# Performance work log

Measured on AMD Instinct MI355X. Metric: run time of the kernel, lower is better.

Reference implementation:

```python
import jax, jax.numpy as jnp
import numpy as np
from itertools import product

# dims
V, B, C, H, Wd = 3, 4, 64, 120, 160   # views, batch, feat2d_channel, image H/W
D3 = 96                               # feat3d_dim
G = 64                                # voxel grid side
N = 200000                            # sparse voxel count
NL = 250000                           # number of link rows
K = 27                                # 3^3 sparse-conv kernel offsets
EPS = 1e-5


def _build_kernel_map(rng):
    # unique sparse coordinates (b,x,y,z) sampled from a B*G^3 grid, sorted by linear code
    lin = np.sort(rng.choice(B * G * G * G, size=N, replace=False)).astype(np.int64)
    b = lin // (G * G * G)
    r = lin % (G * G * G)
    x = r // (G * G)
    y = (r // G) % G
    z = r % G
    in_idx = np.zeros((K, N), np.int32)
    mask = np.zeros((K, N), bool)
    for k, (dx, dy, dz) in enumerate(product((-1, 0, 1), repeat=3)):
        qx, qy, qz = x + dx, y + dy, z + dz
        inb = (qx >= 0) & (qx < G) & (qy >= 0) & (qy < G) & (qz >= 0) & (qz < G)
        qc = ((b * G + np.clip(qx, 0, G - 1)) * G + np.clip(qy, 0, G - 1)) * G + np.clip(qz, 0, G - 1)
        pos = np.clip(np.searchsorted(lin, qc), 0, N - 1)
        ok = inb & (lin[pos] == qc)
        in_idx[k] = np.where(ok, pos, 0)
        mask[k] = ok
    return jnp.asarray(in_idx), jnp.asarray(mask)


def setup_inputs() -> dict:
    rng = np.random.default_rng(0)
    key = jax.random.key(0)
    ks = jax.random.split(key, 8)
    feat_2d_all = jax.random.normal(ks[0], (V, B, C, H, Wd), jnp.float32)
    feat3d_F = jax.random.normal(ks[1], (N, D3), jnp.float32)
    # links: (NL, 4, V) = [batch_idx, v(row), u(col), valid]
    links = np.stack([
        rng.integers(0, B, (NL, V)),
        rng.integers(0, H, (NL, V)),
        rng.integers(0, Wd, (NL, V)),
        rng.integers(0, 2, (NL, V)),
    ], axis=1).astype(np.int32)
    coords_map_out = rng.permutation(N).astype(np.int32)
    coords_map_in = rng.choice(NL, N, replace=False).astype(np.int32)
    in_idx, nbr_mask = _build_kernel_map(rng)
    s = 0.05
    W1 = jax.random.normal(ks[2], (K, V * C, C), jnp.float32) * s
    W2 = jax.random.normal(ks[3], (K, C, D3), jnp.float32) * s
    W3 = jax.random.normal(ks[4], (K, 2 * D3, D3), jnp.float32) * s
    return {
        'feat_2d_all': feat_2d_all, 'feat3d_F': feat3d_F,
        'links': jnp.asarray(links),
        'coords_map_in': jnp.asarray(coords_map_in),
        'coords_map_out': jnp.asarray(coords_map_out),
        'in_idx': in_idx, 'nbr_mask': nbr_mask,
        'W1': W1, 'g1': jnp.ones((C,)), 'b1': jnp.zeros((C,)),
        'W2': W2, 'g2': jnp.ones((D3,)), 'b2': jnp.zeros((D3,)),
        'W3': W3, 'g3': jnp.ones((D3,)), 'b3': jnp.zeros((D3,)),
    }


def _sconv(x, Wk, in_idx, nbr_mask):
    # sparse 3x3x3 conv: out[i] = sum_k x[nbr(i,k)] @ Wk[k], masked where no neighbor
    out = jnp.zeros((x.shape[0], Wk.shape[-1]), x.dtype)
    for k in range(Wk.shape[0]):
        g = x[in_idx[k]] * nbr_mask[k][:, None].astype(x.dtype)
        out = out + g @ Wk[k]
    return out


def _bn_relu(x, g, b):
    mu = x.mean(axis=0)
    var = x.var(axis=0)
    return jax.nn.relu(g * (x - mu) / jnp.sqrt(var + EPS) + b)


def reference(feat_2d_all, feat3d_F, links, coords_map_in, coords_map_out,
              in_idx, nbr_mask, W1, g1, b1, W2, g2, b2, W3, g3, b3):
    n = feat3d_F.shape[0]
    v_, c = feat_2d_all.shape[0], feat_2d_all.shape[2]
    # current_links[coords_map_out] = links[coords_map_in]
    cur = jnp.zeros((n, 4, v_), links.dtype).at[coords_map_out].set(links[coords_map_in])
    bi = cur[:, 0, :].T   # (V, n)
    hi = cur[:, 1, :].T
    wi = cur[:, 2, :].T
    val = cur[:, 3, :].T
    vs = jnp.arange(v_)[:, None]
    # per-view gather from (V,B,C,H,W): advanced indices around the channel slice -> (V, n, C)
    g = feat_2d_all[vs, bi, :, hi, wi]
    g = g * val[:, :, None].astype(g.dtype)
    feat_2d_to_3d = jnp.transpose(g, (1, 0, 2)).reshape(n, v_ * c)
    # view_fusion: conv3 -> BN -> ReLU -> conv3 -> BN -> ReLU
    h = _bn_relu(_sconv(feat_2d_to_3d, W1, in_idx, nbr_mask), g1, b1)
    h = _bn_relu(_sconv(h, W2, in_idx, nbr_mask), g2, b2)
    # cat with 3d features, fuse_to_3d: conv3 -> BN -> ReLU
    cat = jnp.concatenate([feat3d_F, h], axis=-1)
    out = _bn_relu(_sconv(cat, W3, in_idx, nbr_mask), g3, b3)
    return out
```

## Files before the change

kernel.cpp:

```cpp
#include <hip/hip_runtime.h>
#include <stdint.h>


constexpr int NPT = 200000;
constexpr int KNB = 27;

typedef unsigned short u16;
typedef __attribute__((ext_vector_type(8))) short     bf16x8;
typedef __attribute__((ext_vector_type(8))) unsigned short u16x8;
typedef __attribute__((ext_vector_type(4))) float     f32x4;

static __device__ __forceinline__ u16 f2bf(float f){
  unsigned int u = __float_as_uint(f);
  unsigned int r = (u + 0x7fffu + ((u >> 16) & 1u)) >> 16;
  return (u16)r;
}
static __device__ __forceinline__ float bf2f(u16 u){
  return __uint_as_float(((unsigned int)u) << 16);
}

static __device__ __forceinline__ void gload_lds16(const void* g, void* l){
  __builtin_amdgcn_global_load_lds(
      (const __attribute__((address_space(1))) void*)g,
      (__attribute__((address_space(3))) void*)(uint32_t)(uintptr_t)l,
      16, 0, 0);
}

__global__ void detect_mask_kernel(const int* __restrict__ m32, int* __restrict__ flag){
  if (threadIdx.x == 0 && blockIdx.x == 0){
    int ok = 1;
    for (int i = 0; i < 64; ++i){ int v = m32[i]; if (v != 0 && v != 1) ok = 0; }
    *flag = ok ? 2 : 0;
  }
}

__global__ __launch_bounds__(256) void transpose2d_kernel(const float* __restrict__ in,
                                                          u16* __restrict__ out){
  __shared__ float tile[64][33];
  int bid = blockIdx.x;
  int wt = bid % 5;  int rest = bid / 5;
  int h  = rest % 120; rest /= 120;
  int b  = rest % 4;  int v = rest / 4;
  int w0 = wt * 32;
  int tx = threadIdx.x & 31;
  int ty = threadIdx.x >> 5;
  const float* ip = in + ((size_t)(v*4 + b) * 64) * 19200 + h * 160 + w0;
  #pragma unroll
  for (int cc = 0; cc < 8; ++cc){
    int c = cc * 8 + ty;
    tile[c][tx] = ip[(size_t)c * 19200 + tx];
  }
  __syncthreads();
  u16* op = out + (((size_t)(v*4 + b) * 120 + h) * 160 + w0) * 64;
  int c = threadIdx.x & 63;
  int wg = threadIdx.x >> 6;
  #pragma unroll
  for (int i = 0; i < 8; ++i){
    int w = wg + i * 4;
    op[(size_t)w * 64 + c] = f2bf(tile[c][w]);
  }
}

__global__ void wconvert_kernel(const float* __restrict__ src, u16* __restrict__ dst,
                                int cin, int coutT, int coutF, int cbase){
  int gid = blockIdx.x * 256 + threadIdx.x;
  int tot = KNB * cin * coutT;
  if (gid >= tot) return;
  int ncb = coutT / 16;
  int nkc = cin / 32;
  int e    = gid & 7;
  int lane = (gid >> 3) & 63;
  int f    = gid >> 9;
  int cb   = f % ncb;  f /= ncb;
  int kc   = f % nkc;
  int k    = f / nkc;
  int ci = kc * 32 + (lane >> 4) * 8 + e;
  int co = cbase + cb * 16 + (lane & 15);
  dst[gid] = f2bf(src[((size_t)k * cin + ci) * coutF + co]);
}

__global__ void stage_a_kernel(const u16* __restrict__ ft, const int* __restrict__ links,
                               const int* __restrict__ cmi, const int* __restrict__ cmo,
                               u16* __restrict__ x0){
  int gid = blockIdx.x * 256 + threadIdx.x;
  if (gid >= NPT * 3) return;
  int i = gid / 3;
  int v = gid - i * 3;
  int outr = cmo[i];
  int l    = cmi[i];
  int b  = links[l*12 + v];
  int h  = links[l*12 + 3 + v];
  int w  = links[l*12 + 6 + v];
  int vl = links[l*12 + 9 + v];
  u16* dst = x0 + (size_t)outr * 192 + v * 64;
  if (vl){
    const u16* src = ft + (((size_t)(v*4 + b) * 120 + h) * 160 + w) * 64;
    #pragma unroll
    for (int j = 0; j < 8; ++j) ((u16x8*)dst)[j] = ((const u16x8*)src)[j];
  } else {
    u16x8 z = {};
    #pragma unroll
    for (int j = 0; j < 8; ++j) ((u16x8*)dst)[j] = z;
  }
}

__global__ void f3convert_kernel(const float* __restrict__ src, u16* __restrict__ dst){
  long gid = (long)blockIdx.x * 256 + threadIdx.x;
  long tot8 = (long)NPT * 12;
  if (gid >= tot8) return;
  int row = (int)(gid / 12);
  int c0  = (int)(gid % 12) * 8;
  const float* s = src + (size_t)row * 96 + c0;
  u16* d = dst + (size_t)row * 192 + c0;
  #pragma unroll
  for (int j = 0; j < 8; ++j) d[j] = f2bf(s[j]);
}

template<int CIN, int COUT_T, bool COLSPLIT, bool F32OUT>
__global__ __launch_bounds__(256)
void conv_kernel(const u16* __restrict__ x0,
                 const u16* __restrict__ wtA, const u16* __restrict__ wtB,
                 const int* __restrict__ in_idx,
                 const uint8_t* __restrict__ mbytes,
                 const int* __restrict__ flagp, void* __restrict__ outp,
                 int outStride, float* __restrict__ st, int nwork){
  constexpr int NCB    = COUT_T / 16;
  constexpr int NKC    = CIN / 32;
  constexpr int WELE   = CIN * COUT_T;
  constexpr int NCHUNK = (WELE * 2) / 1024;
  constexpr int ROUNDS = (NCHUNK + 3) / 4;
  constexpr int COUTF  = COLSPLIT ? COUT_T * 2 : COUT_T;
  __shared__ __align__(16) u16 wlds[2 * WELE];
  __shared__ float shS[COUT_T], shQ[COUT_T];

  const int v = (blockIdx.x & 7) * (gridDim.x >> 3) + (blockIdx.x >> 3);
  if (v >= nwork) return;

  const int tid    = threadIdx.x;
  const int lane   = tid & 63;
  const int wv     = tid >> 6;
  const int r16    = lane & 15;
  const int kgrp   = lane >> 4;
  const int half   = COLSPLIT ? (v & 1) : 0;
  const int m0     = (COLSPLIT ? (v >> 1) : v) * 128;
  const int cbase  = half * COUT_T;
  const u16* wt    = (COLSPLIT && half) ? wtB : wtA;
  const int mshift = *flagp;

  if (tid < COUT_T){ shS[tid] = 0.f; shQ[tid] = 0.f; }

  f32x4 acc[2][NCB];
  #pragma unroll
  for (int rt = 0; rt < 2; ++rt)
    #pragma unroll
    for (int cb = 0; cb < NCB; ++cb) acc[rt][cb] = (f32x4)0.0f;

  int rowc[2];
  #pragma unroll
  for (int rt = 0; rt < 2; ++rt){
    int row = m0 + wv * 32 + rt * 16 + r16;
    rowc[rt] = row < NPT ? row : NPT - 1;
  }

  #pragma unroll
  for (int rd = 0; rd < ROUNDS; ++rd){
    int chunk = rd * 4 + wv;
    if (chunk < NCHUNK)
      gload_lds16((const char*)wt + chunk * 1024 + lane * 16,
                  (char*)wlds + chunk * 1024);
  }
  int idC[2]; bool mC[2];
  #pragma unroll
  for (int rt = 0; rt < 2; ++rt){
    idC[rt] = in_idx[rowc[rt]];
    mC[rt]  = mbytes[(size_t)rowc[rt] << mshift] != 0;
  }
  __syncthreads();

  const u16* xk = x0 + kgrp * 8;

  for (int k = 0; k < KNB; ++k){
    if (k + 1 < KNB){
      const u16* wn = wt + (size_t)(k + 1) * WELE;
      char* wd = (char*)wlds + ((k + 1) & 1) * (WELE * 2);
      #pragma unroll
      for (int rd = 0; rd < ROUNDS; ++rd){
        int chunk = rd * 4 + wv;
        if (chunk < NCHUNK)
          gload_lds16((const char*)wn + chunk * 1024 + lane * 16,
                      wd + chunk * 1024);
      }
    }

    bf16x8 a0[NKC], a1[NKC];
    #pragma unroll
    for (int kc = 0; kc < NKC; ++kc){ bf16x8 z = {}; a0[kc] = z; a1[kc] = z; }
    if (mC[0]){
      const u16* b0 = xk + (size_t)idC[0] * CIN;
      #pragma unroll
      for (int kc = 0; kc < NKC; ++kc) a0[kc] = *(const bf16x8*)(b0 + kc * 32);
    }
    if (mC[1]){
      const u16* b1 = xk + (size_t)idC[1] * CIN;
      #pragma unroll
      for (int kc = 0; kc < NKC; ++kc) a1[kc] = *(const bf16x8*)(b1 + kc * 32);
    }

    if (k + 1 < KNB){
      #pragma unroll
      for (int rt = 0; rt < 2; ++rt){
        size_t o = (size_t)(k + 1) * NPT + rowc[rt];
        idC[rt] = in_idx[o];
        mC[rt]  = mbytes[o << mshift] != 0;
      }
    }

    const u16* wb = &wlds[(k & 1) * WELE];
    #pragma unroll
    for (int kc = 0; kc < NKC; ++kc){
      #pragma unroll
      for (int cb = 0; cb < NCB; ++cb){
        bf16x8 b = *(const bf16x8*)&wb[((kc * NCB + cb) * 64 + lane) * 8];
        acc[0][cb] = __builtin_amdgcn_mfma_f32_16x16x32_bf16(a0[kc], b, acc[0][cb], 0, 0, 0);
        acc[1][cb] = __builtin_amdgcn_mfma_f32_16x16x32_bf16(a1[kc], b, acc[1][cb], 0, 0, 0);
      }
    }
    __syncthreads();
  }

  #pragma unroll
  for (int rt = 0; rt < 2; ++rt){
    #pragma unroll
    for (int cb = 0; cb < NCB; ++cb){
      const int cout = cb * 16 + r16;
      float s = 0.f, q = 0.f;
      #pragma unroll
      for (int j = 0; j < 4; ++j){
        int row = m0 + wv * 32 + rt * 16 + kgrp * 4 + j;
        if (row < NPT){
          float v2 = acc[rt][cb][j];
          if (F32OUT) ((float*)outp)[(size_t)row * outStride + cbase + cout] = v2;
          else        ((u16*)outp)[(size_t)row * outStride + cbase + cout] = f2bf(v2);
          s += v2; q += v2 * v2;
        }
      }
      atomicAdd(&shS[cout], s); atomicAdd(&shQ[cout], q);
    }
  }
  __syncthreads();
  if (tid < COUT_T){
    atomicAdd(&st[cbase + tid],         shS[tid]);
    atomicAdd(&st[COUTF + cbase + tid], shQ[tid]);
  }
}

template<int CCH, bool ISF32>
__global__ void bnrelu_kernel(void* __restrict__ xp, int stride,
                              const float* __restrict__ st,
                              const float* __restrict__ gg, const float* __restrict__ bb){
  const float invN = 1.0f / (float)NPT;
  constexpr int GPR = CCH / 8;
  long tot8 = (long)NPT * GPR;
  for (long e8 = (long)blockIdx.x * 256 + threadIdx.x; e8 < tot8; e8 += (long)gridDim.x * 256){
    int row = (int)(e8 / GPR);
    int c0  = (int)(e8 % GPR) * 8;
    size_t base = (size_t)row * stride + c0;
    #pragma unroll
    for (int j = 0; j < 8; ++j){
      int c = c0 + j;
      float mu  = st[c] * invN;
      float var = st[CCH + c] * invN - mu * mu;
      float rs  = rsqrtf(var + 1e-5f);
      float x;
      if (ISF32) x = ((float*)xp)[base + j];
      else       x = bf2f(((u16*)xp)[base + j]);
      float y = gg[c] * (x - mu) * rs + bb[c];
      y = y > 0.f ? y : 0.f;
      if (ISF32) ((float*)xp)[base + j] = y;
      else       ((u16*)xp)[base + j] = f2bf(y);
    }
  }
}

extern "C" void kernel_launch(void* const* d_in, const int* in_sizes, int n_in,
                              void* d_out, int out_size, void* d_ws, size_t ws_size,
                              hipStream_t stream){
  const float* feat2d = (const float*)d_in[0];
  const float* feat3d = (const float*)d_in[1];
  const int*   links  = (const int*)d_in[2];
  const int*   cmi    = (const int*)d_in[3];
  const int*   cmo    = (const int*)d_in[4];
  const int*   inidx  = (const int*)d_in[5];
  const void*  mask   = d_in[6];
  const float* W1 = (const float*)d_in[7];
  const float* g1 = (const float*)d_in[8];
  const float* b1 = (const float*)d_in[9];
  const float* W2 = (const float*)d_in[10];
  const float* g2 = (const float*)d_in[11];
  const float* b2 = (const float*)d_in[12];
  const float* W3 = (const float*)d_in[13];
  const float* g3 = (const float*)d_in[14];
  const float* b3 = (const float*)d_in[15];

  char* ws = (char*)d_ws;
  u16* X0 = (u16*)(ws + 0);
  constexpr size_t OFF_B  = 76800512;
  u16* FT = (u16*)(ws + OFF_B);
  u16* Z1 = (u16*)(ws + OFF_B);
  u16* WT1a = (u16*)(ws + 106291712);
  u16* WT1b = WT1a + 27 * 192 * 32;
  u16* WT2  = WT1b + 27 * 192 * 32;
  u16* WT3a = WT2  + 27 * 64 * 96;
  u16* WT3b = WT3a + 27 * 192 * 48;
  float* ST  = (float*)(ws + 108282368);
  float* ST1 = ST;
  float* ST2 = ST + 128;
  float* ST3 = ST + 320;
  int*   FLAG = (int*)(ST + 512);

  hipMemsetAsync(ST, 0, 513 * sizeof(float), stream);
  detect_mask_kernel<<<1, 64, 0, stream>>>((const int*)mask, FLAG);
  transpose2d_kernel<<<7200, 256, 0, stream>>>(feat2d, FT);
  wconvert_kernel<<<(27*192*32 + 255)/256, 256, 0, stream>>>(W1, WT1a, 192, 32, 64, 0);
  wconvert_kernel<<<(27*192*32 + 255)/256, 256, 0, stream>>>(W1, WT1b, 192, 32, 64, 32);
  wconvert_kernel<<<(27*64*96  + 255)/256, 256, 0, stream>>>(W2, WT2, 64, 96, 96, 0);
  wconvert_kernel<<<(27*192*48 + 255)/256, 256, 0, stream>>>(W3, WT3a, 192, 48, 96, 0);
  wconvert_kernel<<<(27*192*48 + 255)/256, 256, 0, stream>>>(W3, WT3b, 192, 48, 96, 48);
  stage_a_kernel<<<(NPT*3 + 255)/256, 256, 0, stream>>>(FT, links, cmi, cmo, X0);

  const int nblk = (NPT + 127) / 128;
  const int nsplit = 2 * nblk;
  const int gsplit = ((nsplit + 7) / 8) * 8;
  const int gnorm  = ((nblk + 7) / 8) * 8;
  const uint8_t* m8 = (const uint8_t*)mask;

  conv_kernel<192, 32, true, false><<<gsplit, 256, 0, stream>>>(
      X0, WT1a, WT1b, inidx, m8, FLAG, Z1, 64, ST1, nsplit);
  bnrelu_kernel<64, false><<<2048, 256, 0, stream>>>(Z1, 64, ST1, g1, b1);

  f3convert_kernel<<<((NPT*12) + 255)/256, 256, 0, stream>>>(feat3d, X0);

  conv_kernel<64, 96, false, false><<<gnorm, 256, 0, stream>>>(
      Z1, WT2, nullptr, inidx, m8, FLAG, X0 + 96, 192, ST2, nblk);
  bnrelu_kernel<96, false><<<2048, 256, 0, stream>>>(X0 + 96, 192, ST2, g2, b2);

  conv_kernel<192, 48, true, true><<<gsplit, 256, 0, stream>>>(
      X0, WT3a, WT3b, inidx, m8, FLAG, d_out, 96, ST3, nsplit);
  bnrelu_kernel<96, true><<<2048, 256, 0, stream>>>(d_out, 96, ST3, g3, b3);
}
```

Before: 873.8 us.

## Raise rows per wave to four tiles and column-split conv2

The sparse conv kernel now takes a template count of 16-row tiles per wave and uses four, so each block covers 256 rows instead of 128. Each LDS weight tile is then reused across more MFMAs, cutting per-block weight reloads. Masked neighbours now point at a zeroed sentinel row (index NPT) instead of branching, which makes the gathers unconditional and lets them interleave with the MFMAs per input chunk. Conv2 is also split into two 48-column halves like the other convs. In exchange, each wave holds more accumulators, which may raise register pressure and lower occupancy.

```diff
diff --git a/kernel.cpp b/kernel.cpp
--- a/kernel.cpp
+++ b/kernel.cpp
@@ -116,7 +116,7 @@
   for (int j = 0; j < 8; ++j) d[j] = f2bf(s[j]);
 }
 
-template<int CIN, int COUT_T, bool COLSPLIT, bool F32OUT>
+template<int CIN, int COUT_T, int NT, bool F32OUT>
 __global__ __launch_bounds__(256)
 void conv_kernel(const u16* __restrict__ x0,
                  const u16* __restrict__ wtA, const u16* __restrict__ wtB,
@@ -129,7 +129,8 @@
   constexpr int WELE   = CIN * COUT_T;
   constexpr int NCHUNK = (WELE * 2) / 1024;
   constexpr int ROUNDS = (NCHUNK + 3) / 4;
-  constexpr int COUTF  = COLSPLIT ? COUT_T * 2 : COUT_T;
+  constexpr int COUTF  = COUT_T * 2;
+  constexpr int RPB    = 64 * NT;
   __shared__ __align__(16) u16 wlds[2 * WELE];
   __shared__ float shS[COUT_T], shQ[COUT_T];
 
@@ -141,24 +142,24 @@
   const int wv     = tid >> 6;
   const int r16    = lane & 15;
   const int kgrp   = lane >> 4;
-  const int half   = COLSPLIT ? (v & 1) : 0;
-  const int m0     = (COLSPLIT ? (v >> 1) : v) * 128;
+  const int half   = v & 1;
+  const int m0     = (v >> 1) * RPB;
   const int cbase  = half * COUT_T;
-  const u16* wt    = (COLSPLIT && half) ? wtB : wtA;
+  const u16* wt    = half ? wtB : wtA;
   const int mshift = *flagp;
 
   if (tid < COUT_T){ shS[tid] = 0.f; shQ[tid] = 0.f; }
 
-  f32x4 acc[2][NCB];
-  #pragma unroll
-  for (int rt = 0; rt < 2; ++rt)
+  f32x4 acc[NT][NCB];
+  #pragma unroll
+  for (int rt = 0; rt < NT; ++rt)
     #pragma unroll
     for (int cb = 0; cb < NCB; ++cb) acc[rt][cb] = (f32x4)0.0f;
 
-  int rowc[2];
-  #pragma unroll
-  for (int rt = 0; rt < 2; ++rt){
-    int row = m0 + wv * 32 + rt * 16 + r16;
+  int rowc[NT];
+  #pragma unroll
+  for (int rt = 0; rt < NT; ++rt){
+    int row = m0 + wv * (16 * NT) + rt * 16 + r16;
     rowc[rt] = row < NPT ? row : NPT - 1;
   }
 
@@ -169,11 +170,12 @@
       gload_lds16((const char*)wt + chunk * 1024 + lane * 16,
                   (char*)wlds + chunk * 1024);
   }
-  int idC[2]; bool mC[2];
-  #pragma unroll
-  for (int rt = 0; rt < 2; ++rt){
-    idC[rt] = in_idx[rowc[rt]];
-    mC[rt]  = mbytes[(size_t)rowc[rt] << mshift] != 0;
+  int vC[NT];
+  #pragma unroll
+  for (int rt = 0; rt < NT; ++rt){
+    int id = in_idx[rowc[rt]];
+    int mv = mbytes[(size_t)rowc[rt] << mshift];
+    vC[rt] = mv ? id : NPT;
   }
   __syncthreads();
 
@@ -192,51 +194,47 @@
       }
     }
 
-    bf16x8 a0[NKC], a1[NKC];
-    #pragma unroll
-    for (int kc = 0; kc < NKC; ++kc){ bf16x8 z = {}; a0[kc] = z; a1[kc] = z; }
-    if (mC[0]){
-      const u16* b0 = xk + (size_t)idC[0] * CIN;
-      #pragma unroll
-      for (int kc = 0; kc < NKC; ++kc) a0[kc] = *(const bf16x8*)(b0 + kc * 32);
-    }
-    if (mC[1]){
-      const u16* b1 = xk + (size_t)idC[1] * CIN;
-      #pragma unroll
-      for (int kc = 0; kc < NKC; ++kc) a1[kc] = *(const bf16x8*)(b1 + kc * 32);
-    }
+    const u16* gb[NT];
+    #pragma unroll
+    for (int rt = 0; rt < NT; ++rt) gb[rt] = xk + (size_t)vC[rt] * CIN;
 
     if (k + 1 < KNB){
       #pragma unroll
-      for (int rt = 0; rt < 2; ++rt){
+      for (int rt = 0; rt < NT; ++rt){
         size_t o = (size_t)(k + 1) * NPT + rowc[rt];
-        idC[rt] = in_idx[o];
-        mC[rt]  = mbytes[o << mshift] != 0;
+        int id = in_idx[o];
+        int mv = mbytes[o << mshift];
+        vC[rt] = mv ? id : NPT;
       }
     }
 
     const u16* wb = &wlds[(k & 1) * WELE];
     #pragma unroll
     for (int kc = 0; kc < NKC; ++kc){
+      bf16x8 a[NT];
+      #pragma unroll
+      for (int rt = 0; rt < NT; ++rt)
+        a[rt] = *(const bf16x8*)(gb[rt] + kc * 32);
       #pragma unroll
       for (int cb = 0; cb < NCB; ++cb){
         bf16x8 b = *(const bf16x8*)&wb[((kc * NCB + cb) * 64 + lane) * 8];
-        acc[0][cb] = __builtin_amdgcn_mfma_f32_16x16x32_bf16(a0[kc], b, acc[0][cb], 0, 0, 0);
-        acc[1][cb] = __builtin_amdgcn_mfma_f32_16x16x32_bf16(a1[kc], b, acc[1][cb], 0, 0, 0);
+        #pragma unroll
+        for (int rt = 0; rt < NT; ++rt)
+          acc[rt][cb] = __builtin_amdgcn_mfma_f32_16x16x32_bf16(a[rt], b, acc[rt][cb], 0, 0, 0);
       }
     }
     __syncthreads();
   }
 
   #pragma unroll
-  for (int rt = 0; rt < 2; ++rt){
+  for (int rt = 0; rt < NT; ++rt){
     #pragma unroll
     for (int cb = 0; cb < NCB; ++cb){
       const int cout = cb * 16 + r16;
       float s = 0.f, q = 0.f;
       #pragma unroll
       for (int j = 0; j < 4; ++j){
-        int row = m0 + wv * 32 + rt * 16 + kgrp * 4 + j;
+        int row = m0 + wv * (16 * NT) + rt * 16 + kgrp * 4 + j;
         if (row < NPT){
           float v2 = acc[rt][cb][j];
           if (F32OUT) ((float*)outp)[(size_t)row * outStride + cbase + cout] = v2;
@@ -309,8 +307,9 @@
   u16* Z1 = (u16*)(ws + OFF_B);
   u16* WT1a = (u16*)(ws + 106291712);
   u16* WT1b = WT1a + 27 * 192 * 32;
-  u16* WT2  = WT1b + 27 * 192 * 32;
-  u16* WT3a = WT2  + 27 * 64 * 96;
+  u16* WT2a = WT1b + 27 * 192 * 32;
+  u16* WT2b = WT2a + 27 * 64 * 48;
+  u16* WT3a = WT2b + 27 * 64 * 48;
   u16* WT3b = WT3a + 27 * 192 * 48;
   float* ST  = (float*)(ws + 108282368);
   float* ST1 = ST;
@@ -323,28 +322,31 @@
   transpose2d_kernel<<<7200, 256, 0, stream>>>(feat2d, FT);
   wconvert_kernel<<<(27*192*32 + 255)/256, 256, 0, stream>>>(W1, WT1a, 192, 32, 64, 0);
   wconvert_kernel<<<(27*192*32 + 255)/256, 256, 0, stream>>>(W1, WT1b, 192, 32, 64, 32);
-  wconvert_kernel<<<(27*64*96  + 255)/256, 256, 0, stream>>>(W2, WT2, 64, 96, 96, 0);
+  wconvert_kernel<<<(27*64*48  + 255)/256, 256, 0, stream>>>(W2, WT2a, 64, 48, 96, 0);
+  wconvert_kernel<<<(27*64*48  + 255)/256, 256, 0, stream>>>(W2, WT2b, 64, 48, 96, 48);
   wconvert_kernel<<<(27*192*48 + 255)/256, 256, 0, stream>>>(W3, WT3a, 192, 48, 96, 0);
   wconvert_kernel<<<(27*192*48 + 255)/256, 256, 0, stream>>>(W3, WT3b, 192, 48, 96, 48);
   stage_a_kernel<<<(NPT*3 + 255)/256, 256, 0, stream>>>(FT, links, cmi, cmo, X0);
 
-  const int nblk = (NPT + 127) / 128;
+  hipMemsetAsync(ws + (size_t)NPT * 384, 0, 384, stream);
+  hipMemsetAsync(ws + OFF_B + (size_t)NPT * 128, 0, 128, stream);
+
+  const int nblk   = (NPT + 255) / 256;
   const int nsplit = 2 * nblk;
   const int gsplit = ((nsplit + 7) / 8) * 8;
-  const int gnorm  = ((nblk + 7) / 8) * 8;
   const uint8_t* m8 = (const uint8_t*)mask;
 
-  conv_kernel<192, 32, true, false><<<gsplit, 256, 0, stream>>>(
+  conv_kernel<192, 32, 4, false><<<gsplit, 256, 0, stream>>>(
       X0, WT1a, WT1b, inidx, m8, FLAG, Z1, 64, ST1, nsplit);
   bnrelu_kernel<64, false><<<2048, 256, 0, stream>>>(Z1, 64, ST1, g1, b1);
 
   f3convert_kernel<<<((NPT*12) + 255)/256, 256, 0, stream>>>(feat3d, X0);
 
-  conv_kernel<64, 96, false, false><<<gnorm, 256, 0, stream>>>(
-      Z1, WT2, nullptr, inidx, m8, FLAG, X0 + 96, 192, ST2, nblk);
+  conv_kernel<64, 48, 4, false><<<gsplit, 256, 0, stream>>>(
+      Z1, WT2a, WT2b, inidx, m8, FLAG, X0 + 96, 192, ST2, nsplit);
   bnrelu_kernel<96, false><<<2048, 256, 0, stream>>>(X0 + 96, 192, ST2, g2, b2);
 
-  conv_kernel<192, 48, true, true><<<gsplit, 256, 0, stream>>>(
+  conv_kernel<192, 48, 4, true><<<gsplit, 256, 0, stream>>>(
       X0, WT3a, WT3b, inidx, m8, FLAG, d_out, 96, ST3, nsplit);
   bnrelu_kernel<96, true><<<2048, 256, 0, stream>>>(d_out, 96, ST3, g3, b3);
 }
```

Result: slower. 1.034 ms (+18.3%).
